# Performance work log

Hardware: AMD Instinct MI355X
Metric: run time of the kernel (lower is better)

## Reference

```python
import jax, jax.numpy as jnp
import numpy as np

N_QUBITS = 8
LATENT = 8
DEPTH = 2


def _ry(state, q, c, s):
    # Apply RY(theta) on qubit q. RY = [[cos(t/2), -sin(t/2)], [sin(t/2), cos(t/2)]].
    # state: (B,) + (2,)*N_QUBITS, purely real (H|0> + real gates keep amplitudes real).
    ax = 1 + q
    a = jnp.take(state, 0, axis=ax)
    b = jnp.take(state, 1, axis=ax)
    return jnp.stack([c * a - s * b, s * a + c * b], axis=ax)


def _cnot(state, cq, tq):
    # CNOT with control cq, target tq: flip target bit where control == 1.
    cax = 1 + cq
    s0 = jnp.take(state, 0, axis=cax)
    s1 = jnp.take(state, 1, axis=cax)
    tax = 1 + tq - (1 if tq > cq else 0)  # target axis after removing control axis
    s1 = jnp.flip(s1, axis=tax)
    return jnp.stack([s0, s1], axis=cax)


def vqc(angles, qw):
    # angles: (B, N_QUBITS) per-sample RY embedding angles; qw: (DEPTH, N_QUBITS).
    B = angles.shape[0]
    n = N_QUBITS
    # H on every qubit of |0...0> gives the uniform real state 2^(-n/2).
    state = jnp.full((B,) + (2,) * n, 2.0 ** (-n / 2), dtype=angles.dtype)
    half = angles * 0.5
    c_all, s_all = jnp.cos(half), jnp.sin(half)
    bshape = (B,) + (1,) * (n - 1)
    for q in range(n):
        state = _ry(state, q, c_all[:, q].reshape(bshape), s_all[:, q].reshape(bshape))
    for k in range(qw.shape[0]):
        for i in range(0, n - 1, 2):
            state = _cnot(state, i, i + 1)
        for i in range(1, n - 1, 2):
            state = _cnot(state, i, i + 1)
        hw = qw[k] * 0.5
        cw, sw = jnp.cos(hw), jnp.sin(hw)
        for q in range(n):
            state = _ry(state, q, cw[q], sw[q])
    probs = state * state  # real amplitudes -> |amp|^2
    exps = []
    for q in range(n):  # <Z_q> = P(bit_q=0) - P(bit_q=1); n_class == n
        axes = tuple(ax for ax in range(1, n + 1) if ax != q + 1)
        m = probs.sum(axis=axes)  # (B, 2)
        exps.append(m[:, 0] - m[:, 1])
    return jnp.stack(exps, axis=1)  # (B, n)


def setup_inputs() -> dict:
    key = jax.random.key(0)
    ks = jax.random.split(key, 11)
    B, S, A = 32768, 8, 4
    return {
        "x": jax.random.normal(ks[0], (B, S), jnp.float32),
        "W_pi1": jax.random.normal(ks[1], (LATENT, S), jnp.float32) * 0.1,
        "b_pi1": jax.random.normal(ks[2], (LATENT,), jnp.float32) * 0.1,
        "qw_pi": jax.random.normal(ks[3], (DEPTH, N_QUBITS), jnp.float32) * 0.01,
        "W_pi2": jax.random.normal(ks[4], (A, LATENT), jnp.float32) * 0.1,
        "b_pi2": jax.random.normal(ks[5], (A,), jnp.float32) * 0.1,
        "W_v1": jax.random.normal(ks[6], (LATENT, S), jnp.float32) * 0.1,
        "b_v1": jax.random.normal(ks[7], (LATENT,), jnp.float32) * 0.1,
        "qw_v": jax.random.normal(ks[8], (DEPTH, N_QUBITS), jnp.float32) * 0.01,
        "W_v2": jax.random.normal(ks[9], (1, LATENT), jnp.float32) * 0.1,
        "b_v2": jax.random.normal(ks[10], (1,), jnp.float32) * 0.1,
    }


def reference(x, W_pi1, b_pi1, qw_pi, W_pi2, b_pi2, W_v1, b_v1, qw_v, W_v2, b_v2):
    pi1 = jnp.tanh(x @ W_pi1.T + b_pi1)
    pi1 = jnp.tanh(vqc(pi1, qw_pi))
    logits = pi1 @ W_pi2.T + b_pi2
    v1 = jnp.tanh(x @ W_v1.T + b_v1)
    v1 = jnp.tanh(vqc(v1, qw_v))
    values = v1 @ W_v2.T + b_v2
    return logits, values
```

## Files before the change

kernel.cpp:

```cpp
#include <hip/hip_runtime.h>

#define BTOT 32768
#define INV2PI 0.15915494309189535f

namespace ct {
constexpr int PMUL[4][4] = {{0,1,2,3},{1,0,3,2},{2,3,0,1},{3,2,1,0}};
constexpr int PPH [4][4] = {{0,0,0,0},{0,0,1,3},{0,3,0,1},{0,1,3,0}};

constexpr unsigned A_STR[8] = {0x3u, 0xFu, 0x3Fu, 0xF0u, 0x3F0u, 0xF00u, 0x3F00u, 0xF000u};
constexpr unsigned B_STR[8] = {0x5u, 0x54u, 0x50u, 0x540u, 0x500u, 0x5400u, 0x5000u, 0x4000u};

struct Terms {
    int n; int w; int supp[3];
    float sgn[8]; unsigned char sbits[8]; unsigned char xm[8]; unsigned char zm[8];
};

constexpr Terms gen(int q, bool xpart) {
    Terms T{};
    const unsigned base = xpart ? B_STR[q] : A_STR[q];
    T.w = 0;
    for (int j = 0; j < 8; ++j)
        if ((base >> (2*j)) & 3u) { T.supp[T.w] = j; T.w++; }
    T.n = 0;
    for (int b = 0; b < (1 << T.w); ++b) {
        unsigned str = 0; int ph = 0; float sg = 1.0f;
        for (int i = 0; i < T.w; ++i) {
            const int j = T.supp[i];
            const int pj = (base >> (2*j)) & 3;
            const bool sbr = ((b >> i) & 1) != 0;
            unsigned f = 0;
            if (pj == 3) { f = sbr ? B_STR[j] : A_STR[j]; if (sbr) sg = -sg; }
            else         { f = sbr ? A_STR[j] : B_STR[j]; }
            unsigned r = 0;
            for (int k = 0; k < 8; ++k) {
                const int pa = (str >> (2*k)) & 3, pb = (f >> (2*k)) & 3;
                r |= (unsigned)PMUL[pa][pb] << (2*k);
                ph = (ph + PPH[pa][pb]) & 3;
            }
            str = r;
        }
        bool dead = false; unsigned xm = 0, zm = 0;
        for (int k = 0; k < 8; ++k) {
            const int p = (str >> (2*k)) & 3;
            if (p == 2) dead = true;
            else if (p == 1) xm |= 1u << k;
            else if (p == 3) zm |= 1u << k;
        }
        if (ph & 1) dead = true;
        if (dead) continue;
        if (ph == 2) sg = -sg;
        T.sgn[T.n] = sg; T.sbits[T.n] = (unsigned char)b;
        T.xm[T.n] = (unsigned char)xm; T.zm[T.n] = (unsigned char)zm;
        T.n++;
    }
    return T;
}

constexpr Terms TA[8] = {gen(0,false),gen(1,false),gen(2,false),gen(3,false),
                         gen(4,false),gen(5,false),gen(6,false),gen(7,false)};
constexpr Terms TB[8] = {gen(0,true),gen(1,true),gen(2,true),gen(3,true),
                         gen(4,true),gen(5,true),gen(6,true),gen(7,true)};

constexpr unsigned suppmask(unsigned str) {
    unsigned m = 0;
    for (int j = 0; j < 8; ++j) if ((str >> (2*j)) & 3u) m |= 1u << j;
    return m;
}
template<int W>
constexpr unsigned c1mask() {
    return suppmask(A_STR[2*W]) | suppmask(B_STR[2*W])
         | suppmask(A_STR[2*W+1]) | suppmask(B_STR[2*W+1]);
}
}

__device__ __forceinline__ float ftanh(float x) {
    float e = __builtin_amdgcn_exp2f(x * 2.8853900817779268f);
    return (e - 1.0f) * __builtin_amdgcn_rcpf(e + 1.0f);
}
__device__ __forceinline__ float fcos(float x) { return __builtin_amdgcn_cosf(x * INV2PI); }
__device__ __forceinline__ float fsin(float x) { return __builtin_amdgcn_sinf(x * INV2PI); }

template<int Q>
__device__ __forceinline__ float eval_q(const float c1[8], const float s1[8],
                                        const float xv[8], const float zv[8],
                                        float c2, float s2)
{
    float EA = 0.0f;
    #pragma unroll
    for (int t = 0; t < 8; ++t) {
        if (t < ct::TA[Q].n) {
            float cf = ct::TA[Q].sgn[t];
            #pragma unroll
            for (int i = 0; i < 3; ++i)
                if (i < ct::TA[Q].w)
                    cf *= ((ct::TA[Q].sbits[t] >> i) & 1) ? s1[ct::TA[Q].supp[i]]
                                                          : c1[ct::TA[Q].supp[i]];
            #pragma unroll
            for (int j = 0; j < 8; ++j) {
                if ((ct::TA[Q].xm[t] >> j) & 1) cf *= xv[j];
                if ((ct::TA[Q].zm[t] >> j) & 1) cf *= zv[j];
            }
            EA += cf;
        }
    }
    float EB = 0.0f;
    #pragma unroll
    for (int t = 0; t < 8; ++t) {
        if (t < ct::TB[Q].n) {
            float cf = ct::TB[Q].sgn[t];
            #pragma unroll
            for (int i = 0; i < 3; ++i)
                if (i < ct::TB[Q].w)
                    cf *= ((ct::TB[Q].sbits[t] >> i) & 1) ? s1[ct::TB[Q].supp[i]]
                                                          : c1[ct::TB[Q].supp[i]];
            #pragma unroll
            for (int j = 0; j < 8; ++j) {
                if ((ct::TB[Q].xm[t] >> j) & 1) cf *= xv[j];
                if ((ct::TB[Q].zm[t] >> j) & 1) cf *= zv[j];
            }
            EB += cf;
        }
    }
    return fmaf(c2, EA, -(s2 * EB));
}

template<int W>
__device__ __forceinline__ void pair_phase(
    const float* __restrict__ x, const float* __restrict__ W1,
    const float* __restrict__ b1, const float* __restrict__ qw,
    int lane, int s, float2 (*xz)[64], float (*ybuf)[64])
{
    constexpr int j0 = 2*W, j1 = 2*W + 1;

    const float4* xr = (const float4*)(x + s * 8);
    const float4 xa = xr[0], xb = xr[1];
    float a0 = b1[j0], a1 = b1[j1];
    a0 = fmaf(xa.x, W1[j0*8+0], a0); a0 = fmaf(xa.y, W1[j0*8+1], a0);
    a0 = fmaf(xa.z, W1[j0*8+2], a0); a0 = fmaf(xa.w, W1[j0*8+3], a0);
    a0 = fmaf(xb.x, W1[j0*8+4], a0); a0 = fmaf(xb.y, W1[j0*8+5], a0);
    a0 = fmaf(xb.z, W1[j0*8+6], a0); a0 = fmaf(xb.w, W1[j0*8+7], a0);
    a1 = fmaf(xa.x, W1[j1*8+0], a1); a1 = fmaf(xa.y, W1[j1*8+1], a1);
    a1 = fmaf(xa.z, W1[j1*8+2], a1); a1 = fmaf(xa.w, W1[j1*8+3], a1);
    a1 = fmaf(xb.x, W1[j1*8+4], a1); a1 = fmaf(xb.y, W1[j1*8+5], a1);
    a1 = fmaf(xb.z, W1[j1*8+6], a1); a1 = fmaf(xb.w, W1[j1*8+7], a1);
    const float th0 = ftanh(a0), th1 = ftanh(a1);
    float2 e0; e0.x = fcos(th0); e0.y = -fsin(th0);
    float2 e1; e1.x = fcos(th1); e1.y = -fsin(th1);
    xz[j0][lane] = e0;
    xz[j1][lane] = e1;
    __syncthreads();

    constexpr unsigned m = ct::c1mask<W>();
    float c1[8], s1[8];
    #pragma unroll
    for (int j = 0; j < 8; ++j) {
        if ((m >> j) & 1) { c1[j] = fcos(qw[j]); s1[j] = fsin(qw[j]); }
    }
    const float c2a = fcos(qw[8+j0]), s2a = fsin(qw[8+j0]);
    const float c2b = fcos(qw[8+j1]), s2b = fsin(qw[8+j1]);

    float xv[8], zv[8];
    #pragma unroll
    for (int j = 0; j < 8; ++j) {
        const float2 t = xz[j][lane];
        xv[j] = t.x; zv[j] = t.y;
    }

    const float y0 = ftanh(eval_q<j0>(c1, s1, xv, zv, c2a, s2a));
    const float y1 = ftanh(eval_q<j1>(c1, s1, xv, zv, c2b, s2b));
    ybuf[j0][lane] = y0;
    ybuf[j1][lane] = y1;
}

__global__ __launch_bounds__(256) void vqc_net(
    const float* __restrict__ x,
    const float* __restrict__ W_pi1, const float* __restrict__ b_pi1,
    const float* __restrict__ qw_pi,
    const float* __restrict__ W_pi2, const float* __restrict__ b_pi2,
    const float* __restrict__ W_v1, const float* __restrict__ b_v1,
    const float* __restrict__ qw_v,
    const float* __restrict__ W_v2, const float* __restrict__ b_v2,
    float* __restrict__ out)
{
    __shared__ float2 xz[8][64];
    __shared__ float  ybuf[8][64];
    __shared__ float4 obuf[64];

    const int tid = threadIdx.x;
    const int lane = tid & 63;
    const int w = tid >> 6;
    const int item = blockIdx.x * 64 + lane;
    const int branch = item >> 15;
    const int s = item & (BTOT - 1);

    const float* W1 = branch ? W_v1 : W_pi1;
    const float* b1 = branch ? b_v1 : b_pi1;
    const float* qw = branch ? qw_v : qw_pi;

    switch (w) {
        case 0:  pair_phase<0>(x, W1, b1, qw, lane, s, xz, ybuf); break;
        case 1:  pair_phase<1>(x, W1, b1, qw, lane, s, xz, ybuf); break;
        case 2:  pair_phase<2>(x, W1, b1, qw, lane, s, xz, ybuf); break;
        default: pair_phase<3>(x, W1, b1, qw, lane, s, xz, ybuf); break;
    }
    __syncthreads();

    if (branch == 0) {
        float o = b_pi2[w];
        #pragma unroll
        for (int j = 0; j < 8; ++j) o = fmaf(ybuf[j][lane], W_pi2[w*8+j], o);
        ((float*)&obuf[lane])[w] = o;
        __syncthreads();
        if (w == 0) *(float4*)(out + s * 4) = obuf[lane];
    } else {
        if (w == 0) {
            float o = b_v2[0];
            #pragma unroll
            for (int j = 0; j < 8; ++j) o = fmaf(ybuf[j][lane], W_v2[j], o);
            out[4 * BTOT + s] = o;
        }
    }
}

extern "C" void kernel_launch(void* const* d_in, const int* in_sizes, int n_in,
                              void* d_out, int out_size, void* d_ws, size_t ws_size,
                              hipStream_t stream) {
    const float* x     = (const float*)d_in[0];
    const float* W_pi1 = (const float*)d_in[1];
    const float* b_pi1 = (const float*)d_in[2];
    const float* qw_pi = (const float*)d_in[3];
    const float* W_pi2 = (const float*)d_in[4];
    const float* b_pi2 = (const float*)d_in[5];
    const float* W_v1  = (const float*)d_in[6];
    const float* b_v1  = (const float*)d_in[7];
    const float* qw_v  = (const float*)d_in[8];
    const float* W_v2  = (const float*)d_in[9];
    const float* b_v2  = (const float*)d_in[10];
    float* out = (float*)d_out;

    const int blocks = (2 * BTOT) / 64;
    vqc_net<<<blocks, 256, 0, stream>>>(
        x, W_pi1, b_pi1, qw_pi, W_pi2, b_pi2,
        W_v1, b_v1, qw_v, W_v2, b_v2, out);
}
```

Measured before the change: 9.464 us.

## Split per-qubit work across eight waves per block instead of four

Each block now uses 512 threads (8 wavefronts), and each wave embeds and evaluates a single qubit rather than a pair. This halves the serial per-thread work and raises the number of waves available to hide latency. In exchange, every lane in every wave reloads x, the per-wave cos/sin setup of the weights is duplicated more, and the larger blocks may lower residency or add barrier cost.

```diff
diff --git a/kernel.cpp b/kernel.cpp
--- a/kernel.cpp
+++ b/kernel.cpp
@@ -66,11 +66,8 @@
     for (int j = 0; j < 8; ++j) if ((str >> (2*j)) & 3u) m |= 1u << j;
     return m;
 }
-template<int W>
-constexpr unsigned c1mask() {
-    return suppmask(A_STR[2*W]) | suppmask(B_STR[2*W])
-         | suppmask(A_STR[2*W+1]) | suppmask(B_STR[2*W+1]);
-}
+template<int Q>
+constexpr unsigned qmask() { return suppmask(A_STR[Q]) | suppmask(B_STR[Q]); }
 }
 
 __device__ __forceinline__ float ftanh(float x) {
@@ -124,55 +121,37 @@
     return fmaf(c2, EA, -(s2 * EB));
 }
 
-template<int W>
-__device__ __forceinline__ void pair_phase(
-    const float* __restrict__ x, const float* __restrict__ W1,
-    const float* __restrict__ b1, const float* __restrict__ qw,
-    int lane, int s, float2 (*xz)[64], float (*ybuf)[64])
-{
-    constexpr int j0 = 2*W, j1 = 2*W + 1;
-
-    const float4* xr = (const float4*)(x + s * 8);
-    const float4 xa = xr[0], xb = xr[1];
-    float a0 = b1[j0], a1 = b1[j1];
-    a0 = fmaf(xa.x, W1[j0*8+0], a0); a0 = fmaf(xa.y, W1[j0*8+1], a0);
-    a0 = fmaf(xa.z, W1[j0*8+2], a0); a0 = fmaf(xa.w, W1[j0*8+3], a0);
-    a0 = fmaf(xb.x, W1[j0*8+4], a0); a0 = fmaf(xb.y, W1[j0*8+5], a0);
-    a0 = fmaf(xb.z, W1[j0*8+6], a0); a0 = fmaf(xb.w, W1[j0*8+7], a0);
-    a1 = fmaf(xa.x, W1[j1*8+0], a1); a1 = fmaf(xa.y, W1[j1*8+1], a1);
-    a1 = fmaf(xa.z, W1[j1*8+2], a1); a1 = fmaf(xa.w, W1[j1*8+3], a1);
-    a1 = fmaf(xb.x, W1[j1*8+4], a1); a1 = fmaf(xb.y, W1[j1*8+5], a1);
-    a1 = fmaf(xb.z, W1[j1*8+6], a1); a1 = fmaf(xb.w, W1[j1*8+7], a1);
-    const float th0 = ftanh(a0), th1 = ftanh(a1);
-    float2 e0; e0.x = fcos(th0); e0.y = -fsin(th0);
-    float2 e1; e1.x = fcos(th1); e1.y = -fsin(th1);
-    xz[j0][lane] = e0;
-    xz[j1][lane] = e1;
-    __syncthreads();
-
-    constexpr unsigned m = ct::c1mask<W>();
+template<int Q>
+__device__ __forceinline__ void embed_q(
+    const float4 xa, const float4 xb, const float* __restrict__ W1,
+    const float* __restrict__ b1, int lane, float2 (*xz)[64])
+{
+    float a = b1[Q];
+    a = fmaf(xa.x, W1[Q*8+0], a); a = fmaf(xa.y, W1[Q*8+1], a);
+    a = fmaf(xa.z, W1[Q*8+2], a); a = fmaf(xa.w, W1[Q*8+3], a);
+    a = fmaf(xb.x, W1[Q*8+4], a); a = fmaf(xb.y, W1[Q*8+5], a);
+    a = fmaf(xb.z, W1[Q*8+6], a); a = fmaf(xb.w, W1[Q*8+7], a);
+    const float th = ftanh(a);
+    float2 e; e.x = fcos(th); e.y = -fsin(th);
+    xz[Q][lane] = e;
+}
+
+template<int Q>
+__device__ __forceinline__ void eval_phase(
+    const float* __restrict__ qw, int lane,
+    const float xv[8], const float zv[8], float (*ybuf)[64])
+{
+    constexpr unsigned m = ct::qmask<Q>();
     float c1[8], s1[8];
     #pragma unroll
     for (int j = 0; j < 8; ++j) {
         if ((m >> j) & 1) { c1[j] = fcos(qw[j]); s1[j] = fsin(qw[j]); }
     }
-    const float c2a = fcos(qw[8+j0]), s2a = fsin(qw[8+j0]);
-    const float c2b = fcos(qw[8+j1]), s2b = fsin(qw[8+j1]);
-
-    float xv[8], zv[8];
-    #pragma unroll
-    for (int j = 0; j < 8; ++j) {
-        const float2 t = xz[j][lane];
-        xv[j] = t.x; zv[j] = t.y;
-    }
-
-    const float y0 = ftanh(eval_q<j0>(c1, s1, xv, zv, c2a, s2a));
-    const float y1 = ftanh(eval_q<j1>(c1, s1, xv, zv, c2b, s2b));
-    ybuf[j0][lane] = y0;
-    ybuf[j1][lane] = y1;
-}
-
-__global__ __launch_bounds__(256) void vqc_net(
+    const float c2 = fcos(qw[8+Q]), s2 = fsin(qw[8+Q]);
+    ybuf[Q][lane] = ftanh(eval_q<Q>(c1, s1, xv, zv, c2, s2));
+}
+
+__global__ __launch_bounds__(512) void vqc_net(
     const float* __restrict__ x,
     const float* __restrict__ W_pi1, const float* __restrict__ b_pi1,
     const float* __restrict__ qw_pi,
@@ -197,19 +176,47 @@
     const float* b1 = branch ? b_v1 : b_pi1;
     const float* qw = branch ? qw_v : qw_pi;
 
+    const float4* xr = (const float4*)(x + s * 8);
+    const float4 xa = xr[0], xb = xr[1];
+
     switch (w) {
-        case 0:  pair_phase<0>(x, W1, b1, qw, lane, s, xz, ybuf); break;
-        case 1:  pair_phase<1>(x, W1, b1, qw, lane, s, xz, ybuf); break;
-        case 2:  pair_phase<2>(x, W1, b1, qw, lane, s, xz, ybuf); break;
-        default: pair_phase<3>(x, W1, b1, qw, lane, s, xz, ybuf); break;
+        case 0: embed_q<0>(xa, xb, W1, b1, lane, xz); break;
+        case 1: embed_q<1>(xa, xb, W1, b1, lane, xz); break;
+        case 2: embed_q<2>(xa, xb, W1, b1, lane, xz); break;
+        case 3: embed_q<3>(xa, xb, W1, b1, lane, xz); break;
+        case 4: embed_q<4>(xa, xb, W1, b1, lane, xz); break;
+        case 5: embed_q<5>(xa, xb, W1, b1, lane, xz); break;
+        case 6: embed_q<6>(xa, xb, W1, b1, lane, xz); break;
+        default: embed_q<7>(xa, xb, W1, b1, lane, xz); break;
     }
     __syncthreads();
 
+    float xv[8], zv[8];
+    #pragma unroll
+    for (int j = 0; j < 8; ++j) {
+        const float2 t = xz[j][lane];
+        xv[j] = t.x; zv[j] = t.y;
+    }
+
+    switch (w) {
+        case 0: eval_phase<0>(qw, lane, xv, zv, ybuf); break;
+        case 1: eval_phase<1>(qw, lane, xv, zv, ybuf); break;
+        case 2: eval_phase<2>(qw, lane, xv, zv, ybuf); break;
+        case 3: eval_phase<3>(qw, lane, xv, zv, ybuf); break;
+        case 4: eval_phase<4>(qw, lane, xv, zv, ybuf); break;
+        case 5: eval_phase<5>(qw, lane, xv, zv, ybuf); break;
+        case 6: eval_phase<6>(qw, lane, xv, zv, ybuf); break;
+        default: eval_phase<7>(qw, lane, xv, zv, ybuf); break;
+    }
+    __syncthreads();
+
     if (branch == 0) {
-        float o = b_pi2[w];
-        #pragma unroll
-        for (int j = 0; j < 8; ++j) o = fmaf(ybuf[j][lane], W_pi2[w*8+j], o);
-        ((float*)&obuf[lane])[w] = o;
+        if (w < 4) {
+            float o = b_pi2[w];
+            #pragma unroll
+            for (int j = 0; j < 8; ++j) o = fmaf(ybuf[j][lane], W_pi2[w*8+j], o);
+            ((float*)&obuf[lane])[w] = o;
+        }
         __syncthreads();
         if (w == 0) *(float4*)(out + s * 4) = obuf[lane];
     } else {
@@ -239,7 +246,7 @@
     float* out = (float*)d_out;
 
     const int blocks = (2 * BTOT) / 64;
-    vqc_net<<<blocks, 256, 0, stream>>>(
+    vqc_net<<<blocks, 512, 0, stream>>>(
         x, W_pi1, b_pi1, qw_pi, W_pi2, b_pi2,
         W_v1, b_v1, qw_v, W_v2, b_v2, out);
 }
```

Result: slower. 11.89 us (+25.6%).
